# Optimization experiments

Hardware: AMD Instinct MI355X
Metric: run time of the kernel (lower is better)

The kernel has to match this reference:

```python
import jax, jax.numpy as jnp
import numpy as np

B, S, D = 2, 2048, 1024
H, DH = 16, 64
FF = 4 * D
EPS = 1e-5
SCALE = 1.0 / np.sqrt(DH)


def setup_inputs() -> dict:
    key = jax.random.key(0)
    ks = jax.random.split(key, 8)
    std = 0.02
    return {
        "x": jax.random.normal(ks[0], (B, S, D), jnp.float32),
        "ln1_g": jnp.ones((D,), jnp.float32),
        "ln1_b": jnp.zeros((D,), jnp.float32),
        "w_qkv": jax.random.normal(ks[1], (D, 3 * H * DH), jnp.float32) * std,
        "b_qkv": jnp.zeros((3 * H * DH,), jnp.float32),
        "w_ao": jax.random.normal(ks[2], (H * DH, D), jnp.float32) * std,
        "b_ao": jnp.zeros((D,), jnp.float32),
        "ln2_g": jnp.ones((D,), jnp.float32),
        "ln2_b": jnp.zeros((D,), jnp.float32),
        "w_fc": jax.random.normal(ks[3], (D, FF), jnp.float32) * std,
        "b_fc": jnp.zeros((FF,), jnp.float32),
        "w_proj": jax.random.normal(ks[4], (FF, D), jnp.float32) * std,
        "b_proj": jnp.zeros((D,), jnp.float32),
    }


def _layernorm(x, g, b):
    mu = jnp.mean(x, axis=-1, keepdims=True)
    var = jnp.mean(jnp.square(x - mu), axis=-1, keepdims=True)
    return (x - mu) * jax.lax.rsqrt(var + EPS) * g + b


def reference(x, ln1_g, ln1_b, w_qkv, b_qkv, w_ao, b_ao,
              ln2_g, ln2_b, w_fc, b_fc, w_proj, b_proj):
    # pre-LN attention
    h = _layernorm(x, ln1_g, ln1_b)
    qkv = h @ w_qkv + b_qkv                      # [B,S,3*H*DH]
    q, k, v = jnp.split(qkv, 3, axis=-1)
    def heads(t):                                 # [B,S,H*DH] -> [B,H,S,DH]
        return t.reshape(B, S, H, DH).transpose(0, 2, 1, 3)
    q, k, v = heads(q), heads(k), heads(v)
    scores = jnp.einsum("bhsd,bhtd->bhst", q, k) * SCALE  # full [B,H,S,S]
    probs = jax.nn.softmax(scores, axis=-1)
    attn = jnp.einsum("bhst,bhtd->bhsd", probs, v)        # [B,H,S,DH]
    attn = attn.transpose(0, 2, 1, 3).reshape(B, S, H * DH)
    attn = attn @ w_ao + b_ao
    x = x + attn
    # pre-LN MLP (exact erf GELU, matches nn.GELU())
    h = _layernorm(x, ln2_g, ln2_b)
    h = jax.nn.gelu(h @ w_fc + b_fc, approximate=False)
    h = h @ w_proj + b_proj
    return x + h
```

## Files before the change

### kernel.cpp

```cpp
#include <hip/hip_runtime.h>
#include <hip/hip_bf16.h>

using short8 = __attribute__((ext_vector_type(8))) short;
using f32x4  = __attribute__((ext_vector_type(4))) float;

#define DEV __device__ __forceinline__

DEV unsigned short f2b(float f) {
  union { float f; unsigned u; } cv; cv.f = f;
  unsigned r = (cv.u + 0x7fffu + ((cv.u >> 16) & 1u)) >> 16;
  return (unsigned short)r;
}

typedef const __attribute__((address_space(1))) unsigned int* gp1;
typedef __attribute__((address_space(3))) unsigned int* lp3;
DEV void gl16(const void* g, void* l) {
  __builtin_amdgcn_global_load_lds((gp1)g, (lp3)l, 16, 0, 0);
}

__global__ void k_tcvt(const float* __restrict__ src, unsigned short* __restrict__ dst,
                       int K, int N) {
  __shared__ float tile[32][33];
  int n0 = blockIdx.x * 32, k0 = blockIdx.y * 32;
  int tx = threadIdx.x, ty = threadIdx.y;
#pragma unroll
  for (int j = 0; j < 4; ++j)
    tile[ty + j * 8][tx] = src[(size_t)(k0 + ty + j * 8) * N + (n0 + tx)];
  __syncthreads();
#pragma unroll
  for (int j = 0; j < 4; ++j)
    dst[(size_t)(n0 + ty + j * 8) * K + (k0 + tx)] = f2b(tile[tx][ty + j * 8]);
}

__global__ void k_tv(const unsigned short* __restrict__ src, unsigned short* __restrict__ dst) {
  __shared__ unsigned short tile[32][33];
  int d0 = blockIdx.x * 32, s0 = blockIdx.y * 32;
  size_t base = (size_t)blockIdx.z * 2048 * 64;
  int tx = threadIdx.x, ty = threadIdx.y;
#pragma unroll
  for (int j = 0; j < 4; ++j)
    tile[ty + j * 8][tx] = src[base + (size_t)(s0 + ty + j * 8) * 64 + (d0 + tx)];
  __syncthreads();
#pragma unroll
  for (int j = 0; j < 4; ++j)
    dst[base + (size_t)(d0 + ty + j * 8) * 2048 + (s0 + tx)] = tile[tx][ty + j * 8];
}

__global__ __launch_bounds__(256) void k_ln(const float* __restrict__ x,
                                            const float* __restrict__ g,
                                            const float* __restrict__ b,
                                            unsigned short* __restrict__ y) {
  int row = blockIdx.x, tid = threadIdx.x;
  float4 v = reinterpret_cast<const float4*>(x + (size_t)row * 1024)[tid];
  float s  = v.x + v.y + v.z + v.w;
  float s2 = v.x * v.x + v.y * v.y + v.z * v.z + v.w * v.w;
#pragma unroll
  for (int m = 1; m < 64; m <<= 1) { s += __shfl_xor(s, m); s2 += __shfl_xor(s2, m); }
  __shared__ float ps[8];
  int w = tid >> 6;
  if ((tid & 63) == 0) { ps[w] = s; ps[4 + w] = s2; }
  __syncthreads();
  s  = ps[0] + ps[1] + ps[2] + ps[3];
  s2 = ps[4] + ps[5] + ps[6] + ps[7];
  float mu   = s * (1.0f / 1024.0f);
  float var  = fmaxf(s2 * (1.0f / 1024.0f) - mu * mu, 0.f);
  float rstd = rsqrtf(var + 1e-5f);
  float4 gv = reinterpret_cast<const float4*>(g)[tid];
  float4 bv = reinterpret_cast<const float4*>(b)[tid];
  ushort4 o;
  o.x = f2b((v.x - mu) * rstd * gv.x + bv.x);
  o.y = f2b((v.y - mu) * rstd * gv.y + bv.y);
  o.z = f2b((v.z - mu) * rstd * gv.z + bv.z);
  o.w = f2b((v.w - mu) * rstd * gv.w + bv.w);
  reinterpret_cast<ushort4*>(y + (size_t)row * 1024)[tid] = o;
}

enum { EPI_QKV = 0, EPI_RESID = 1, EPI_GELU = 2 };

template <int EPI>
__global__ __launch_bounds__(512, 2) void k_gemm256(
    const unsigned short* __restrict__ A, const unsigned short* __restrict__ BT,
    const float* __restrict__ bias, int M, int N, int K,
    unsigned short* __restrict__ outb,
    unsigned short* __restrict__ qb, unsigned short* __restrict__ kb,
    unsigned short* __restrict__ vb) {
  __shared__ __align__(16) unsigned short Abuf[2][256][64];
  __shared__ __align__(16) unsigned short Bbuf[2][256][64];
  int nx = gridDim.x, nwg = nx * gridDim.y;
  int w0 = blockIdx.y * nx + blockIdx.x;
  int id = (w0 & 7) * (nwg >> 3) + (w0 >> 3);
  int bx = id % nx, by = id / nx;
  int m0 = by * 256, n0 = bx * 256;
  int tid = threadIdx.x;
  int lane = tid & 63, wid = tid >> 6;
  int wm = wid >> 2, wn = wid & 3;
  int l15 = lane & 15, g = lane >> 4;
  int swl = l15 & 7;
  int lrow = lane >> 3;
  int lchunk = (lane & 7) ^ lrow;
  const unsigned short* Asrc = A  + (size_t)(m0 + wid * 32 + lrow) * K + lchunk * 8;
  const unsigned short* Bsrc = BT + (size_t)(n0 + wid * 32 + lrow) * K + lchunk * 8;
  auto stage = [&](int buf, int k0) {
#pragma unroll
    for (int i = 0; i < 4; ++i)
      gl16(Asrc + k0 + (size_t)i * 8 * K, &Abuf[buf][wid * 32 + i * 8][0]);
#pragma unroll
    for (int i = 0; i < 4; ++i)
      gl16(Bsrc + k0 + (size_t)i * 8 * K, &Bbuf[buf][wid * 32 + i * 8][0]);
  };
  f32x4 acc[8][4] = {};
  int nt = K >> 6;
  stage(0, 0);
  stage(1, 64);
  asm volatile("s_waitcnt vmcnt(8)" ::: "memory");
  __builtin_amdgcn_sched_barrier(0);
  __builtin_amdgcn_s_barrier();
  int cur = 0;
  for (int t = 0; t < nt; ++t) {
    const unsigned short (*As)[64] = Abuf[cur];
    const unsigned short (*Bs)[64] = Bbuf[cur];
    short8 a0[8], b0[4], a1[8], b1[4];
#pragma unroll
    for (int mi = 0; mi < 8; ++mi)
      a0[mi] = *reinterpret_cast<const short8*>(&As[wm * 128 + mi * 16 + l15][(g ^ swl) * 8]);
#pragma unroll
    for (int ni = 0; ni < 4; ++ni)
      b0[ni] = *reinterpret_cast<const short8*>(&Bs[wn * 64 + ni * 16 + l15][(g ^ swl) * 8]);
    __builtin_amdgcn_s_setprio(1);
#pragma unroll
    for (int mi = 0; mi < 8; ++mi)
#pragma unroll
      for (int ni = 0; ni < 4; ++ni)
        acc[mi][ni] = __builtin_amdgcn_mfma_f32_16x16x32_bf16(a0[mi], b0[ni], acc[mi][ni], 0, 0, 0);
    __builtin_amdgcn_s_setprio(0);
#pragma unroll
    for (int mi = 0; mi < 8; ++mi)
      a1[mi] = *reinterpret_cast<const short8*>(&As[wm * 128 + mi * 16 + l15][((4 + g) ^ swl) * 8]);
#pragma unroll
    for (int ni = 0; ni < 4; ++ni)
      b1[ni] = *reinterpret_cast<const short8*>(&Bs[wn * 64 + ni * 16 + l15][((4 + g) ^ swl) * 8]);
    asm volatile("s_waitcnt lgkmcnt(0)" ::: "memory");
    __builtin_amdgcn_sched_barrier(0);
    __builtin_amdgcn_s_barrier();
    __builtin_amdgcn_sched_barrier(0);
    if (t + 2 < nt) stage(cur, (t + 2) << 6);
    __builtin_amdgcn_s_setprio(1);
#pragma unroll
    for (int mi = 0; mi < 8; ++mi)
#pragma unroll
      for (int ni = 0; ni < 4; ++ni)
        acc[mi][ni] = __builtin_amdgcn_mfma_f32_16x16x32_bf16(a1[mi], b1[ni], acc[mi][ni], 0, 0, 0);
    __builtin_amdgcn_s_setprio(0);
    if (t + 2 < nt) {
      asm volatile("s_waitcnt vmcnt(8)" ::: "memory");
    } else if (t + 1 < nt) {
      asm volatile("s_waitcnt vmcnt(0)" ::: "memory");
    }
    __builtin_amdgcn_sched_barrier(0);
    __builtin_amdgcn_s_barrier();
    cur ^= 1;
  }
#pragma unroll
  for (int mi = 0; mi < 8; ++mi) {
#pragma unroll
    for (int ni = 0; ni < 4; ++ni) {
      int row0 = m0 + wm * 128 + mi * 16 + g * 4;
      int col  = n0 + wn * 64 + ni * 16 + l15;
      float bcol = bias[col];
#pragma unroll
      for (int j = 0; j < 4; ++j) {
        int r = row0 + j;
        float vv = acc[mi][ni][j] + bcol;
        if (EPI == EPI_QKV) {
          int which = col >> 10;
          int hc = col & 1023;
          int h = hc >> 6, d = hc & 63;
          int bb = r >> 11, ss = r & 2047;
          size_t idx = (((size_t)(bb * 16 + h)) * 2048 + ss) * 64 + d;
          unsigned short bv_ = f2b(which == 0 ? vv * 0.18033688011112042f : vv);
          if (which == 0)      qb[idx] = bv_;
          else if (which == 1) kb[idx] = bv_;
          else                 vb[idx] = bv_;
        } else {
          float ge = 0.5f * vv * (1.0f + erff(vv * 0.70710678118654752f));
          outb[(size_t)r * N + col] = f2b(ge);
        }
      }
    }
  }
}

__global__ __launch_bounds__(512) void k_gemm512(
    const unsigned short* __restrict__ A, const unsigned short* __restrict__ BT,
    const float* __restrict__ bias, int M, int N, int K,
    float* __restrict__ outf, const float* __restrict__ resid) {
  __shared__ __align__(16) unsigned short Abuf[2][64][64];
  __shared__ __align__(16) unsigned short Bbuf[2][128][64];
  int nx = gridDim.x, nwg = nx * gridDim.y;
  int w0 = blockIdx.y * nx + blockIdx.x;
  int id = (w0 & 7) * (nwg >> 3) + (w0 >> 3);
  int bx = id % nx, by = id / nx;
  int m0 = by * 64, n0 = bx * 128;
  int tid = threadIdx.x;
  int lane = tid & 63, wid = tid >> 6;
  int wm = wid >> 2, wn = wid & 3;
  int l15 = lane & 15, g = lane >> 4;
  int swl = l15 & 7;
  int lrow = lane >> 3;
  int lchunk = (lane & 7) ^ lrow;
  const unsigned short* Asrc = A  + (size_t)(m0 + wid * 8 + lrow) * K + lchunk * 8;
  const unsigned short* Bsrc = BT + (size_t)(n0 + wid * 16 + lrow) * K + lchunk * 8;
  auto stage = [&](int buf, int k0) {
    gl16(Asrc + k0, &Abuf[buf][wid * 8][0]);
#pragma unroll
    for (int i = 0; i < 2; ++i)
      gl16(Bsrc + k0 + (size_t)i * 8 * K, &Bbuf[buf][wid * 16 + i * 8][0]);
  };
  f32x4 acc[2][2] = {};
  int nt = K >> 6;
  stage(0, 0);
  stage(1, 64);
  asm volatile("s_waitcnt vmcnt(3)" ::: "memory");
  __builtin_amdgcn_sched_barrier(0);
  __builtin_amdgcn_s_barrier();
  int cur = 0;
  for (int t = 0; t < nt; ++t) {
    const unsigned short (*As)[64] = Abuf[cur];
    const unsigned short (*Bs)[64] = Bbuf[cur];
    short8 a0[2], b0[2], a1[2], b1[2];
#pragma unroll
    for (int mi = 0; mi < 2; ++mi)
      a0[mi] = *reinterpret_cast<const short8*>(&As[wm * 32 + mi * 16 + l15][(g ^ swl) * 8]);
#pragma unroll
    for (int ni = 0; ni < 2; ++ni)
      b0[ni] = *reinterpret_cast<const short8*>(&Bs[wn * 32 + ni * 16 + l15][(g ^ swl) * 8]);
    __builtin_amdgcn_s_setprio(1);
#pragma unroll
    for (int mi = 0; mi < 2; ++mi)
#pragma unroll
      for (int ni = 0; ni < 2; ++ni)
        acc[mi][ni] = __builtin_amdgcn_mfma_f32_16x16x32_bf16(a0[mi], b0[ni], acc[mi][ni], 0, 0, 0);
    __builtin_amdgcn_s_setprio(0);
#pragma unroll
    for (int mi = 0; mi < 2; ++mi)
      a1[mi] = *reinterpret_cast<const short8*>(&As[wm * 32 + mi * 16 + l15][((4 + g) ^ swl) * 8]);
#pragma unroll
    for (int ni = 0; ni < 2; ++ni)
      b1[ni] = *reinterpret_cast<const short8*>(&Bs[wn * 32 + ni * 16 + l15][((4 + g) ^ swl) * 8]);
    asm volatile("s_waitcnt lgkmcnt(0)" ::: "memory");
    __builtin_amdgcn_sched_barrier(0);
    __builtin_amdgcn_s_barrier();
    __builtin_amdgcn_sched_barrier(0);
    if (t + 2 < nt) stage(cur, (t + 2) << 6);
    __builtin_amdgcn_s_setprio(1);
#pragma unroll
    for (int mi = 0; mi < 2; ++mi)
#pragma unroll
      for (int ni = 0; ni < 2; ++ni)
        acc[mi][ni] = __builtin_amdgcn_mfma_f32_16x16x32_bf16(a1[mi], b1[ni], acc[mi][ni], 0, 0, 0);
    __builtin_amdgcn_s_setprio(0);
    if (t + 2 < nt) {
      asm volatile("s_waitcnt vmcnt(3)" ::: "memory");
    } else if (t + 1 < nt) {
      asm volatile("s_waitcnt vmcnt(0)" ::: "memory");
    }
    __builtin_amdgcn_sched_barrier(0);
    __builtin_amdgcn_s_barrier();
    cur ^= 1;
  }
#pragma unroll
  for (int mi = 0; mi < 2; ++mi) {
#pragma unroll
    for (int ni = 0; ni < 2; ++ni) {
      int row0 = m0 + wm * 32 + mi * 16 + g * 4;
      int col  = n0 + wn * 32 + ni * 16 + l15;
      float bcol = bias[col];
#pragma unroll
      for (int j = 0; j < 4; ++j) {
        size_t idx = (size_t)(row0 + j) * N + col;
        outf[idx] = acc[mi][ni][j] + bcol + resid[idx];
      }
    }
  }
}

__global__ __launch_bounds__(256) void k_attn(
    const unsigned short* __restrict__ qb, const unsigned short* __restrict__ kb,
    const unsigned short* __restrict__ vt, unsigned short* __restrict__ attn_out) {
  __shared__ __align__(16) unsigned short Ks[64][64];
  __shared__ __align__(16) unsigned short Vs[64][64];
  __shared__ __align__(16) unsigned short Plds[4][16][72];
  int bh = blockIdx.y;
  int b = bh >> 4, h = bh & 15;
  int tid = threadIdx.x;
  int lane = tid & 63, wid = tid >> 6;
  int l15 = lane & 15, g = lane >> 4;
  int q0 = blockIdx.x * 64 + wid * 16;
  const unsigned short* Qb = qb + (size_t)bh * 2048 * 64;
  const unsigned short* Kb = kb + (size_t)bh * 2048 * 64;
  const unsigned short* Vt = vt + (size_t)bh * 64 * 2048;
  short8 qf0 = *reinterpret_cast<const short8*>(&Qb[(size_t)(q0 + l15) * 64 + g * 8]);
  short8 qf1 = *reinterpret_cast<const short8*>(&Qb[(size_t)(q0 + l15) * 64 + 32 + g * 8]);
  float mj = -1e30f, lj = 0.f;
  f32x4 o[4] = {};
  int sr  = wid * 16 + (lane >> 3);
  int scn = (lane & 7) ^ (sr & 7);
  int swl = l15 & 7;
  for (int t0 = 0; t0 < 2048; t0 += 64) {
    __syncthreads();
    gl16(Kb + (size_t)(t0 + sr) * 64 + scn * 8,       &Ks[wid * 16][0]);
    gl16(Kb + (size_t)(t0 + sr + 8) * 64 + scn * 8,   &Ks[wid * 16 + 8][0]);
    gl16(Vt + (size_t)sr * 2048 + t0 + scn * 8,       &Vs[wid * 16][0]);
    gl16(Vt + (size_t)(sr + 8) * 2048 + t0 + scn * 8, &Vs[wid * 16 + 8][0]);
    __syncthreads();
    f32x4 scv[4];
#pragma unroll
    for (int kk = 0; kk < 4; ++kk) {
      short8 kf0 = *reinterpret_cast<const short8*>(&Ks[kk * 16 + l15][(g ^ swl) * 8]);
      short8 kf1 = *reinterpret_cast<const short8*>(&Ks[kk * 16 + l15][((4 + g) ^ swl) * 8]);
      f32x4 z = {};
      z = __builtin_amdgcn_mfma_f32_16x16x32_bf16(kf0, qf0, z, 0, 0, 0);
      scv[kk] = __builtin_amdgcn_mfma_f32_16x16x32_bf16(kf1, qf1, z, 0, 0, 0);
    }
    float mx = -1e30f;
#pragma unroll
    for (int kk = 0; kk < 4; ++kk)
#pragma unroll
      for (int j = 0; j < 4; ++j) mx = fmaxf(mx, scv[kk][j]);
    mx = fmaxf(mx, __shfl_xor(mx, 16));
    mx = fmaxf(mx, __shfl_xor(mx, 32));
    bool skip = __all(mx <= mj + 8.0f);
    float mnew = skip ? mj : fmaxf(mj, mx);
    float p[16];
    float ts = 0.f;
#pragma unroll
    for (int kk = 0; kk < 4; ++kk)
#pragma unroll
      for (int j = 0; j < 4; ++j) {
        float pv = __builtin_amdgcn_exp2f(scv[kk][j] - mnew);
        p[kk * 4 + j] = pv;
        ts += pv;
      }
    ts += __shfl_xor(ts, 16);
    ts += __shfl_xor(ts, 32);
    if (!skip) {
      float ef = __builtin_amdgcn_exp2f(mj - mnew);
      int sb = 20 * g;
      float e0 = __shfl(ef, sb + 0), e1 = __shfl(ef, sb + 1);
      float e2 = __shfl(ef, sb + 2), e3 = __shfl(ef, sb + 3);
#pragma unroll
      for (int ct = 0; ct < 4; ++ct) {
        o[ct][0] *= e0; o[ct][1] *= e1; o[ct][2] *= e2; o[ct][3] *= e3;
      }
      lj = lj * ef + ts;
      mj = mnew;
    } else {
      lj += ts;
    }
#pragma unroll
    for (int kk = 0; kk < 4; ++kk) {
      unsigned r0, r1;
      asm("v_cvt_pk_bf16_f32 %0, %1, %2" : "=v"(r0) : "v"(p[kk * 4 + 0]), "v"(p[kk * 4 + 1]));
      asm("v_cvt_pk_bf16_f32 %0, %1, %2" : "=v"(r1) : "v"(p[kk * 4 + 2]), "v"(p[kk * 4 + 3]));
      unsigned long long w = (unsigned long long)r0 | ((unsigned long long)r1 << 32);
      *reinterpret_cast<unsigned long long*>(&Plds[wid][l15][kk * 16 + g * 4]) = w;
    }
    short8 pf0 = *reinterpret_cast<const short8*>(&Plds[wid][l15][g * 8]);
    short8 pf1 = *reinterpret_cast<const short8*>(&Plds[wid][l15][32 + g * 8]);
#pragma unroll
    for (int ct = 0; ct < 4; ++ct) {
      short8 vf0 = *reinterpret_cast<const short8*>(&Vs[ct * 16 + l15][(g ^ swl) * 8]);
      short8 vf1 = *reinterpret_cast<const short8*>(&Vs[ct * 16 + l15][((4 + g) ^ swl) * 8]);
      o[ct] = __builtin_amdgcn_mfma_f32_16x16x32_bf16(pf0, vf0, o[ct], 0, 0, 0);
      o[ct] = __builtin_amdgcn_mfma_f32_16x16x32_bf16(pf1, vf1, o[ct], 0, 0, 0);
    }
  }
  float invq = 1.0f / lj;
  int sb = 20 * g;
  float i0 = __shfl(invq, sb + 0), i1 = __shfl(invq, sb + 1);
  float i2 = __shfl(invq, sb + 2), i3 = __shfl(invq, sb + 3);
  float iv[4] = {i0, i1, i2, i3};
#pragma unroll
  for (int j = 0; j < 4; ++j) {
    size_t t = (size_t)b * 2048 + (q0 + g * 4 + j);
#pragma unroll
    for (int ct = 0; ct < 4; ++ct)
      attn_out[t * 1024 + h * 64 + ct * 16 + l15] = f2b(o[ct][j] * iv[j]);
  }
}

extern "C" void kernel_launch(void* const* d_in, const int* in_sizes, int n_in,
                              void* d_out, int out_size, void* d_ws, size_t ws_size,
                              hipStream_t stream) {
  (void)in_sizes; (void)n_in; (void)out_size; (void)ws_size;
  const float* x      = (const float*)d_in[0];
  const float* ln1_g  = (const float*)d_in[1];
  const float* ln1_b  = (const float*)d_in[2];
  const float* w_qkv  = (const float*)d_in[3];
  const float* b_qkv  = (const float*)d_in[4];
  const float* w_ao   = (const float*)d_in[5];
  const float* b_ao   = (const float*)d_in[6];
  const float* ln2_g  = (const float*)d_in[7];
  const float* ln2_b  = (const float*)d_in[8];
  const float* w_fc   = (const float*)d_in[9];
  const float* b_fc   = (const float*)d_in[10];
  const float* w_proj = (const float*)d_in[11];
  const float* b_proj = (const float*)d_in[12];
  float* out = (float*)d_out;

  char* ws = (char*)d_ws;
  size_t o = 0;
  auto nxt = [&](size_t bytes) { void* p = ws + o; o += (bytes + 255) & ~(size_t)255; return p; };
  unsigned short* wT_qkv  = (unsigned short*)nxt((size_t)3072 * 1024 * 2);
  unsigned short* wT_ao   = (unsigned short*)nxt((size_t)1024 * 1024 * 2);
  unsigned short* wT_fc   = (unsigned short*)nxt((size_t)4096 * 1024 * 2);
  unsigned short* wT_proj = (unsigned short*)nxt((size_t)1024 * 4096 * 2);
  unsigned short* h_ln    = (unsigned short*)nxt((size_t)4096 * 1024 * 2);
  unsigned short* qbuf    = (unsigned short*)nxt((size_t)4096 * 1024 * 2);
  unsigned short* kbuf    = (unsigned short*)nxt((size_t)4096 * 1024 * 2);
  unsigned short* vbuf    = (unsigned short*)nxt((size_t)4096 * 1024 * 2);
  unsigned short* vtb     = (unsigned short*)nxt((size_t)4096 * 1024 * 2);
  float*          out1    = (float*)nxt((size_t)4096 * 1024 * 4);
  unsigned short* fc_buf  = qbuf;
  unsigned short* attn_o  = vbuf;

  dim3 b32(32, 8, 1);
  k_tcvt<<<dim3(96, 32), b32, 0, stream>>>(w_qkv, wT_qkv, 1024, 3072);
  k_tcvt<<<dim3(32, 32), b32, 0, stream>>>(w_ao, wT_ao, 1024, 1024);
  k_tcvt<<<dim3(128, 32), b32, 0, stream>>>(w_fc, wT_fc, 1024, 4096);
  k_tcvt<<<dim3(32, 128), b32, 0, stream>>>(w_proj, wT_proj, 4096, 1024);

  k_ln<<<4096, 256, 0, stream>>>(x, ln1_g, ln1_b, h_ln);
  k_gemm256<EPI_QKV><<<dim3(12, 16), 512, 0, stream>>>(h_ln, wT_qkv, b_qkv, 4096, 3072, 1024,
                                                       nullptr, qbuf, kbuf, vbuf);
  k_tv<<<dim3(2, 64, 32), b32, 0, stream>>>(vbuf, vtb);
  k_attn<<<dim3(32, 32), 256, 0, stream>>>(qbuf, kbuf, vtb, attn_o);
  k_gemm512<<<dim3(8, 64), 512, 0, stream>>>(attn_o, wT_ao, b_ao, 4096, 1024, 1024,
                                             out1, x);
  k_ln<<<4096, 256, 0, stream>>>(out1, ln2_g, ln2_b, h_ln);
  k_gemm256<EPI_GELU><<<dim3(16, 16), 512, 0, stream>>>(h_ln, wT_fc, b_fc, 4096, 4096, 1024,
                                                        fc_buf, nullptr, nullptr, nullptr);
  k_gemm512<<<dim3(8, 64), 512, 0, stream>>>(fc_buf, wT_proj, b_proj, 4096, 1024, 4096,
                                             out, out1);
}
```

Before: 248.4 us.

## Restructure 256x256 GEMM mainloop into quadrant ping-pong with split staging

```diff
diff --git a/kernel.cpp b/kernel.cpp
--- a/kernel.cpp
+++ b/kernel.cpp
@@ -96,70 +96,113 @@
   int wm = wid >> 2, wn = wid & 3;
   int l15 = lane & 15, g = lane >> 4;
   int swl = l15 & 7;
-  int lrow = lane >> 3;
-  int lchunk = (lane & 7) ^ lrow;
-  const unsigned short* Asrc = A  + (size_t)(m0 + wid * 32 + lrow) * K + lchunk * 8;
-  const unsigned short* Bsrc = BT + (size_t)(n0 + wid * 32 + lrow) * K + lchunk * 8;
-  auto stage = [&](int buf, int k0) {
-#pragma unroll
-    for (int i = 0; i < 4; ++i)
-      gl16(Asrc + k0 + (size_t)i * 8 * K, &Abuf[buf][wid * 32 + i * 8][0]);
-#pragma unroll
-    for (int i = 0; i < 4; ++i)
-      gl16(Bsrc + k0 + (size_t)i * 8 * K, &Bbuf[buf][wid * 32 + i * 8][0]);
+  int lr8 = lane >> 3;
+  int sch = (lane & 7) ^ lr8;
+  auto stA = [&](int buf, int t, int half) {
+#pragma unroll
+    for (int i = 0; i < 2; ++i) {
+      int r = half * 128 + wid * 16 + i * 8;
+      gl16(A + (size_t)(m0 + r + lr8) * K + (t << 6) + sch * 8, &Abuf[buf][r][0]);
+    }
+  };
+  auto stB = [&](int buf, int t, int half) {
+#pragma unroll
+    for (int i = 0; i < 2; ++i) {
+      int r = half * 128 + wid * 16 + i * 8;
+      gl16(BT + (size_t)(n0 + r + lr8) * K + (t << 6) + sch * 8, &Bbuf[buf][r][0]);
+    }
   };
   f32x4 acc[8][4] = {};
+  short8 afr[4][2], bf0[2][2], bf1[2][2];
+  auto rdA = [&](const unsigned short (*As)[64], int mh) {
+#pragma unroll
+    for (int mi = 0; mi < 4; ++mi) {
+      const unsigned short* rp = &As[wm * 128 + mh * 64 + mi * 16 + l15][0];
+      afr[mi][0] = *reinterpret_cast<const short8*>(&rp[(g ^ swl) * 8]);
+      afr[mi][1] = *reinterpret_cast<const short8*>(&rp[((4 + g) ^ swl) * 8]);
+    }
+  };
+  auto rdB = [&](short8 (&bf)[2][2], const unsigned short (*Bs)[64], int nh) {
+#pragma unroll
+    for (int ni = 0; ni < 2; ++ni) {
+      const unsigned short* rp = &Bs[wn * 64 + nh * 32 + ni * 16 + l15][0];
+      bf[ni][0] = *reinterpret_cast<const short8*>(&rp[(g ^ swl) * 8]);
+      bf[ni][1] = *reinterpret_cast<const short8*>(&rp[((4 + g) ^ swl) * 8]);
+    }
+  };
+  auto quad = [&](short8 (&bf)[2][2], int mh, int nh) {
+    __builtin_amdgcn_s_setprio(1);
+#pragma unroll
+    for (int mi = 0; mi < 4; ++mi)
+#pragma unroll
+      for (int ni = 0; ni < 2; ++ni) {
+        acc[mh * 4 + mi][nh * 2 + ni] =
+            __builtin_amdgcn_mfma_f32_16x16x32_bf16(afr[mi][0], bf[ni][0], acc[mh * 4 + mi][nh * 2 + ni], 0, 0, 0);
+        acc[mh * 4 + mi][nh * 2 + ni] =
+            __builtin_amdgcn_mfma_f32_16x16x32_bf16(afr[mi][1], bf[ni][1], acc[mh * 4 + mi][nh * 2 + ni], 0, 0, 0);
+      }
+    __builtin_amdgcn_s_setprio(0);
+  };
+#define LGKM0 do { asm volatile("s_waitcnt lgkmcnt(0)" ::: "memory"); __builtin_amdgcn_sched_barrier(0); } while (0)
+#define BAR   __builtin_amdgcn_s_barrier()
   int nt = K >> 6;
-  stage(0, 0);
-  stage(1, 64);
-  asm volatile("s_waitcnt vmcnt(8)" ::: "memory");
+  stB(0, 0, 0); stB(0, 0, 1); stA(0, 0, 0); stA(0, 0, 1);
+  stB(1, 1, 0); stB(1, 1, 1);
+  asm volatile("s_waitcnt vmcnt(4)" ::: "memory");
   __builtin_amdgcn_sched_barrier(0);
-  __builtin_amdgcn_s_barrier();
-  int cur = 0;
-  for (int t = 0; t < nt; ++t) {
-    const unsigned short (*As)[64] = Abuf[cur];
-    const unsigned short (*Bs)[64] = Bbuf[cur];
-    short8 a0[8], b0[4], a1[8], b1[4];
-#pragma unroll
-    for (int mi = 0; mi < 8; ++mi)
-      a0[mi] = *reinterpret_cast<const short8*>(&As[wm * 128 + mi * 16 + l15][(g ^ swl) * 8]);
-#pragma unroll
-    for (int ni = 0; ni < 4; ++ni)
-      b0[ni] = *reinterpret_cast<const short8*>(&Bs[wn * 64 + ni * 16 + l15][(g ^ swl) * 8]);
-    __builtin_amdgcn_s_setprio(1);
-#pragma unroll
-    for (int mi = 0; mi < 8; ++mi)
-#pragma unroll
-      for (int ni = 0; ni < 4; ++ni)
-        acc[mi][ni] = __builtin_amdgcn_mfma_f32_16x16x32_bf16(a0[mi], b0[ni], acc[mi][ni], 0, 0, 0);
-    __builtin_amdgcn_s_setprio(0);
-#pragma unroll
-    for (int mi = 0; mi < 8; ++mi)
-      a1[mi] = *reinterpret_cast<const short8*>(&As[wm * 128 + mi * 16 + l15][((4 + g) ^ swl) * 8]);
-#pragma unroll
-    for (int ni = 0; ni < 4; ++ni)
-      b1[ni] = *reinterpret_cast<const short8*>(&Bs[wn * 64 + ni * 16 + l15][((4 + g) ^ swl) * 8]);
-    asm volatile("s_waitcnt lgkmcnt(0)" ::: "memory");
+  BAR;
+  for (int t = 0; t < nt; t += 2) {
+    const unsigned short (*A0)[64] = Abuf[0];
+    const unsigned short (*B0)[64] = Bbuf[0];
+    const unsigned short (*A1)[64] = Abuf[1];
+    const unsigned short (*B1)[64] = Bbuf[1];
+    bool s2 = (t + 2 < nt);
+    rdA(A0, 0); rdB(bf0, B0, 0);
+    stA(1, t + 1, 0);
+    BAR; LGKM0;
+    quad(bf0, 0, 0);
+    BAR;
+    rdB(bf1, B0, 1);
+    stA(1, t + 1, 1);
+    BAR; LGKM0;
+    quad(bf1, 0, 1);
+    BAR;
+    rdA(A0, 1);
+    if (s2) stB(0, t + 2, 0);
+    BAR; LGKM0;
+    quad(bf1, 1, 1);
+    BAR;
+    if (s2) stB(0, t + 2, 1);
+    quad(bf0, 1, 0);
+    if (s2) { asm volatile("s_waitcnt vmcnt(4)" ::: "memory"); }
+    else    { asm volatile("s_waitcnt vmcnt(0)" ::: "memory"); }
     __builtin_amdgcn_sched_barrier(0);
-    __builtin_amdgcn_s_barrier();
-    __builtin_amdgcn_sched_barrier(0);
-    if (t + 2 < nt) stage(cur, (t + 2) << 6);
-    __builtin_amdgcn_s_setprio(1);
-#pragma unroll
-    for (int mi = 0; mi < 8; ++mi)
-#pragma unroll
-      for (int ni = 0; ni < 4; ++ni)
-        acc[mi][ni] = __builtin_amdgcn_mfma_f32_16x16x32_bf16(a1[mi], b1[ni], acc[mi][ni], 0, 0, 0);
-    __builtin_amdgcn_s_setprio(0);
-    if (t + 2 < nt) {
-      asm volatile("s_waitcnt vmcnt(8)" ::: "memory");
-    } else if (t + 1 < nt) {
-      asm volatile("s_waitcnt vmcnt(0)" ::: "memory");
-    }
-    __builtin_amdgcn_sched_barrier(0);
-    __builtin_amdgcn_s_barrier();
-    cur ^= 1;
-  }
+    BAR;
+    rdA(A1, 0); rdB(bf0, B1, 0);
+    if (s2) stA(0, t + 2, 0);
+    BAR; LGKM0;
+    quad(bf0, 0, 0);
+    BAR;
+    rdB(bf1, B1, 1);
+    if (s2) stA(0, t + 2, 1);
+    BAR; LGKM0;
+    quad(bf1, 0, 1);
+    BAR;
+    rdA(A1, 1);
+    if (s2) stB(1, t + 3, 0);
+    BAR; LGKM0;
+    quad(bf1, 1, 1);
+    BAR;
+    if (s2) stB(1, t + 3, 1);
+    quad(bf0, 1, 0);
+    if (s2) {
+      asm volatile("s_waitcnt vmcnt(4)" ::: "memory");
+      __builtin_amdgcn_sched_barrier(0);
+    }
+    BAR;
+  }
+#undef LGKM0
+#undef BAR
 #pragma unroll
   for (int mi = 0; mi < 8; ++mi) {
 #pragma unroll
```

Measured after the change: 252.5 us. About the same (+1.6%).
